# Performance work log

Measured on AMD Instinct MI355X. Metric: run time of the kernel, lower is better.

## Reference

```python
import jax, jax.numpy as jnp
import numpy as np

V = 50000        # fine nodes
E = 400000       # edges
NEXT_DIM = 12500 # coarse nodes (nextDim)
B = 2
FIN, FOUT = 64, 128


def setup_inputs() -> dict:
    key = jax.random.key(0)
    ks = jax.random.split(key, 12)
    x = jax.random.normal(ks[0], (B, V, FIN), dtype=jnp.float32)
    adjValue = jax.random.uniform(ks[1], (E,), dtype=jnp.float32)
    edgeOne = jnp.ones((E,), dtype=jnp.float32)
    E_start = jax.random.randint(ks[2], (E,), 0, V, dtype=jnp.int32)
    E_end = jax.random.randint(ks[3], (E,), 0, V, dtype=jnp.int32)
    # avg-pool assignment: each fine node v -> coarse node v//4, weight 1/4
    fine = jnp.arange(V, dtype=jnp.int32)
    avgPoolAsgnIdx = jnp.stack([fine // 4, fine])  # [2, nnz]
    avgPoolAsgnValue = jnp.full((V,), 0.25, dtype=jnp.float32)
    s = 0.05
    W_res = jax.random.normal(ks[4], (FIN, FOUT), dtype=jnp.float32) * s
    b_res = jnp.zeros((FOUT,), dtype=jnp.float32)
    W0_self = jax.random.normal(ks[5], (FIN, FOUT), dtype=jnp.float32) * s
    W0_nb = jax.random.normal(ks[6], (FIN, FOUT), dtype=jnp.float32) * s
    b0 = jnp.zeros((FOUT,), dtype=jnp.float32)
    W1_self = jax.random.normal(ks[7], (FOUT, FOUT), dtype=jnp.float32) * s
    W1_nb = jax.random.normal(ks[8], (FOUT, FOUT), dtype=jnp.float32) * s
    b1 = jnp.zeros((FOUT,), dtype=jnp.float32)
    return {"x": x, "adjValue": adjValue, "edgeOne": edgeOne,
            "E_start": E_start, "E_end": E_end,
            "avgPoolAsgnIdx": avgPoolAsgnIdx, "avgPoolAsgnValue": avgPoolAsgnValue,
            "W_res": W_res, "b_res": b_res,
            "W0_self": W0_self, "W0_nb": W0_nb, "b0": b0,
            "W1_self": W1_self, "W1_nb": W1_nb, "b1": b1}


def _ecc(x, Ws, Wn, b, adjValue, E_start, E_end, deg_inv):
    # Edge-conditioned conv: out_i = x_i Ws + (1/deg_i) * sum_{e: start=i} adj_e * (x_{end(e)} Wn) + b
    Bn, Vn, _ = x.shape
    h = jnp.einsum('bvf,fo->bvo', x, Wn)            # neighbor transform [B,V,Fo]
    ht = h.transpose(1, 0, 2).reshape(Vn, -1)       # [V, B*Fo]
    msg = ht[E_end] * adjValue[:, None]             # gather + edge weight [E, B*Fo]
    agg = jax.ops.segment_sum(msg, E_start, num_segments=Vn)  # scatter-add [V, B*Fo]
    agg = (agg * deg_inv[:, None]).reshape(Vn, Bn, -1).transpose(1, 0, 2)
    return jnp.einsum('bvf,fo->bvo', x, Ws) + agg + b


def _batch_spmm(idx, value, m, x):
    # sparse (m x n) @ x per batch; x: [B, n, F]
    Bn, n, F = x.shape
    xt = x.transpose(1, 0, 2).reshape(n, -1)        # [n, B*F]
    g = xt[idx[1]] * value[:, None]                 # [nnz, B*F]
    out = jax.ops.segment_sum(g, idx[0], num_segments=m)
    return out.reshape(m, Bn, F).transpose(1, 0, 2)


def reference(x, adjValue, edgeOne, E_start, E_end, avgPoolAsgnIdx, avgPoolAsgnValue,
              W_res, b_res, W0_self, W0_nb, b0, W1_self, W1_nb, b1):
    deg = jax.ops.segment_sum(edgeOne, E_start, num_segments=V)
    deg_inv = 1.0 / jnp.maximum(deg, 1.0)
    # residual path: 1x1 conv == per-node linear, then pool
    residual = jnp.einsum('bvf,fo->bvo', x, W_res) + b_res
    residual = _batch_spmm(avgPoolAsgnIdx, avgPoolAsgnValue, NEXT_DIM, residual)
    # main path: ECC -> leaky_relu(0.2) -> ECC -> pool
    out = _ecc(x, W0_self, W0_nb, b0, adjValue, E_start, E_end, deg_inv)
    out = jnp.where(out >= 0, out, 0.2 * out)
    out = _ecc(out, W1_self, W1_nb, b1, adjValue, E_start, E_end, deg_inv)
    out = _batch_spmm(avgPoolAsgnIdx, avgPoolAsgnValue, NEXT_DIM, out)
    return out + residual
```

## Files before the change

kernel.cpp:

```cpp
#include <hip/hip_runtime.h>

#define V_N    50000
#define E_N    400000
#define NEXT_N 12500
#define B_N    2
#define M_ROWS (V_N * B_N)
#define NSBLK  196

typedef float  f32x2  __attribute__((ext_vector_type(2)));
typedef float  f32x4  __attribute__((ext_vector_type(4)));
typedef __bf16 bf16x8 __attribute__((ext_vector_type(8)));
typedef unsigned int u32x2 __attribute__((ext_vector_type(2)));
typedef unsigned int u32x4 __attribute__((ext_vector_type(4)));

__device__ __forceinline__ float bflo(unsigned int u) {
    return __builtin_bit_cast(float, u << 16);
}
__device__ __forceinline__ float bfhi(unsigned int u) {
    return __builtin_bit_cast(float, u & 0xffff0000u);
}
__device__ __forceinline__ unsigned short bf16bits(float f) {
    return __builtin_bit_cast(unsigned short, (__bf16)f);
}

__device__ __forceinline__ void wcvt_one(int idx, int phase,
                                         const float* Wa, const float* Wb, const float* Wc,
                                         unsigned int* dst) {
    int kc = idx >> 11;
    int jj = idx & 3, lane = (idx >> 2) & 63, nt = (idx >> 8) & 7;
    int kk = kc * 32 + ((lane >> 4) * 8) + jj * 2;
    int n  = nt * 16 + (lane & 15);
    const float* Wsrc; int kbase;
    if (phase == 0) {
        if (kk < 64) { Wsrc = Wa; kbase = 0; } else { Wsrc = Wb; kbase = 64; }
    } else {
        if (kk < 128)      { Wsrc = Wa; kbase = 0; }
        else if (kk < 256) { Wsrc = Wb; kbase = 128; }
        else               { Wsrc = Wc; kbase = 256; }
    }
    float w0 = Wsrc[(kk - kbase) * 128 + n];
    float w1 = Wsrc[(kk + 1 - kbase) * 128 + n];
    dst[idx] = ((unsigned int)bf16bits(w1) << 16) | bf16bits(w0);
}

__global__ void prep_kernel(const float* __restrict__ x, unsigned int* __restrict__ xbf,
                            const int* __restrict__ Es, int* __restrict__ degi,
                            const int* __restrict__ poolIdx, const float* __restrict__ poolVal,
                            int* __restrict__ invRow, float* __restrict__ invVal,
                            const float* __restrict__ W0s, const float* __restrict__ W0n,
                            const float* __restrict__ W1s, const float* __restrict__ W1n,
                            const float* __restrict__ Wres,
                            unsigned int* __restrict__ Wc0, unsigned int* __restrict__ Wc1) {
    int blk = blockIdx.x, t = threadIdx.x;
    if (blk < 12500) {
        int i = blk * 256 + t;
        f32x2 p = *(const f32x2*)(x + (size_t)i * 2);
        xbf[i] = ((unsigned int)bf16bits(p[1]) << 16) | bf16bits(p[0]);
    } else if (blk < 14063) {
        int e = (blk - 12500) * 256 + t;
        if (e < E_N) atomicAdd(&degi[Es[e]], 1);
    } else if (blk < 14259) {
        int j = (blk - 14063) * 256 + t;
        if (j < V_N) {
            int c = poolIdx[V_N + j];
            invRow[c] = poolIdx[j];
            invVal[c] = poolVal[j];
        }
    } else if (blk < 14291) {
        wcvt_one((blk - 14259) * 256 + t, 0, W0s, W0n, nullptr, Wc0);
    } else {
        wcvt_one((blk - 14291) * 256 + t, 1, W1s, W1n, Wres, Wc1);
    }
}

__global__ void partial_kernel(const int* __restrict__ degi, int* __restrict__ part) {
    __shared__ int sh[256];
    int t = threadIdx.x, i = blockIdx.x * 256 + t;
    sh[t] = (i < V_N) ? degi[i] : 0;
    __syncthreads();
    for (int off = 128; off > 0; off >>= 1) {
        if (t < off) sh[t] += sh[t + off];
        __syncthreads();
    }
    if (t == 0) part[blockIdx.x] = sh[0];
}

__global__ void scanpart_kernel(const int* __restrict__ part, int* __restrict__ bofs) {
    __shared__ int sh[256];
    int t = threadIdx.x;
    int p = (t < NSBLK) ? part[t] : 0;
    sh[t] = p;
    __syncthreads();
    for (int off = 1; off < 256; off <<= 1) {
        int v = (t >= off) ? sh[t - off] : 0;
        __syncthreads();
        sh[t] += v;
        __syncthreads();
    }
    if (t < NSBLK) bofs[t] = sh[t] - p;
}

__global__ void emit_kernel(const int* __restrict__ degi, const int* __restrict__ bofs,
                            int* __restrict__ cur, float* __restrict__ dinv) {
    __shared__ int sh[256];
    int t = threadIdx.x, i = blockIdx.x * 256 + t;
    int d = (i < V_N) ? degi[i] : 0;
    sh[t] = d;
    __syncthreads();
    for (int off = 1; off < 256; off <<= 1) {
        int v = (t >= off) ? sh[t - off] : 0;
        __syncthreads();
        sh[t] += v;
        __syncthreads();
    }
    if (i < V_N) {
        cur[i] = bofs[blockIdx.x] + sh[t] - d;
        dinv[i] = 1.0f / (float)(d > 1 ? d : 1);
    }
}

__global__ void csr_kernel(const int* __restrict__ Es, const int* __restrict__ Ee,
                           const float* __restrict__ adj, int* __restrict__ cur,
                           int* __restrict__ cdst, float* __restrict__ cval) {
    int e = blockIdx.x * 256 + threadIdx.x;
    if (e < E_N) {
        int pos = atomicAdd(&cur[Es[e]], 1);
        cdst[pos] = Ee[e];
        cval[pos] = adj[e];
    }
}

__global__ __launch_bounds__(256) void agg0_kernel(
    const unsigned int* __restrict__ xbf, const int* __restrict__ cur,
    const int* __restrict__ cdst, const float* __restrict__ cval,
    const float* __restrict__ dinv, unsigned int* __restrict__ AGG0bf) {
    int w = blockIdx.x * 4 + (threadIdx.x >> 6);
    int lane = threadIdx.x & 63;
    int beg = w ? cur[w - 1] : 0;
    int end = cur[w];
    int b = lane >> 5, u = lane & 31;
    const unsigned int* src = xbf + (size_t)b * V_N * 32 + u;
    float s0 = 0.f, s1 = 0.f;
    for (int base = beg; base < end; base += 8) {
        int li = base + (lane & 7);
        bool lv = li < end;
        int dk = lv ? cdst[li] : 0;
        float ak = lv ? cval[li] : 0.0f;
        unsigned int pv[8]; float av[8];
#pragma unroll
        for (int j = 0; j < 8; ++j) {
            int dj = __shfl(dk, j);
            av[j] = __shfl(ak, j);
            pv[j] = src[(size_t)dj * 32];
        }
#pragma unroll
        for (int j = 0; j < 8; ++j) { s0 += av[j] * bflo(pv[j]); s1 += av[j] * bfhi(pv[j]); }
    }
    float dv = dinv[w];
    AGG0bf[((size_t)b * V_N + w) * 32 + u] =
        ((unsigned int)bf16bits(s1 * dv) << 16) | bf16bits(s0 * dv);
}

__global__ __launch_bounds__(256) void agg1_kernel(
    const unsigned int* __restrict__ obf, const int* __restrict__ cur,
    const int* __restrict__ cdst, const float* __restrict__ cval,
    const float* __restrict__ dinv, unsigned int* __restrict__ AGG1bf) {
    int w = blockIdx.x * 4 + (threadIdx.x >> 6);
    int lane = threadIdx.x & 63;
    int beg = w ? cur[w - 1] : 0;
    int end = cur[w];
    int b = lane >> 5;
    int u = (lane & 31) * 2;
    const unsigned int* src = obf + (size_t)b * V_N * 64 + u;
    float s[4] = {0, 0, 0, 0};
    for (int base = beg; base < end; base += 8) {
        int li = base + (lane & 7);
        bool lv = li < end;
        int dk = lv ? cdst[li] : 0;
        float ak = lv ? cval[li] : 0.0f;
        u32x2 pv[8]; float av[8];
#pragma unroll
        for (int j = 0; j < 8; ++j) {
            int dj = __shfl(dk, j);
            av[j] = __shfl(ak, j);
            pv[j] = *(const u32x2*)(src + (size_t)dj * 64);
        }
#pragma unroll
        for (int j = 0; j < 8; ++j) {
            s[0] += av[j] * bflo(pv[j][0]); s[1] += av[j] * bfhi(pv[j][0]);
            s[2] += av[j] * bflo(pv[j][1]); s[3] += av[j] * bfhi(pv[j][1]);
        }
    }
    float dv = dinv[w];
    u32x2 r;
    r[0] = ((unsigned int)bf16bits(s[1] * dv) << 16) | bf16bits(s[0] * dv);
    r[1] = ((unsigned int)bf16bits(s[3] * dv) << 16) | bf16bits(s[2] * dv);
    *(u32x2*)(AGG1bf + ((size_t)b * V_N + w) * 64 + u) = r;
}

template <int PHASE>
__global__ __launch_bounds__(256) void gemm_kernel(
    const unsigned int* __restrict__ xbf, const unsigned int* __restrict__ INbf,
    const unsigned int* __restrict__ AGGbf, const unsigned int* __restrict__ Wcvt,
    const float* __restrict__ bias0, const float* __restrict__ bias1,
    const int* __restrict__ invRow, const float* __restrict__ invVal,
    unsigned short* __restrict__ OUTbf, float* __restrict__ out) {
    constexpr int K  = (PHASE == 0) ? 128 : 320;
    constexpr int KC = K / 32;

    __shared__ unsigned int ldsW[KC * 2048];

    const int tid  = threadIdx.x;
    const int wave = tid >> 6, lane = tid & 63;
    const int m = lane & 15, quad = lane >> 4;

    {
        const u32x4* src4 = (const u32x4*)Wcvt;
        u32x4* dst4 = (u32x4*)ldsW;
#pragma unroll
        for (int it = 0; it < 2 * KC; ++it) dst4[it * 256 + tid] = src4[it * 256 + tid];
    }
    __syncthreads();

    const int rowA  = blockIdx.x * 64 + wave * 16 + m;
    const int rowAc = rowA < M_ROWS ? rowA : M_ROWS - 1;

    f32x4 acc[8];
#pragma unroll
    for (int i = 0; i < 8; ++i)
#pragma unroll
        for (int r = 0; r < 4; ++r) acc[i][r] = 0.0f;

#pragma unroll
    for (int kc = 0; kc < KC; ++kc) {
        int k0 = kc * 32 + quad * 8;
        const unsigned int* abase;
        if (PHASE == 0) {
            abase = (k0 < 64) ? xbf + (size_t)rowAc * 32 + (k0 >> 1)
                              : AGGbf + (size_t)rowAc * 32 + ((k0 - 64) >> 1);
        } else {
            if (k0 < 128)      abase = INbf + (size_t)rowAc * 64 + (k0 >> 1);
            else if (k0 < 256) abase = AGGbf + (size_t)rowAc * 64 + ((k0 - 128) >> 1);
            else               abase = xbf + (size_t)rowAc * 32 + ((k0 - 256) >> 1);
        }
        bf16x8 av = __builtin_bit_cast(bf16x8, *(const u32x4*)abase);
#pragma unroll
        for (int nt = 0; nt < 8; ++nt) {
            bf16x8 bv = __builtin_bit_cast(
                bf16x8, *(const u32x4*)&ldsW[(kc * 8 + nt) * 256 + lane * 4]);
            acc[nt] = __builtin_amdgcn_mfma_f32_16x16x32_bf16(av, bv, acc[nt], 0, 0, 0);
        }
    }

    const int rowq = blockIdx.x * 64 + wave * 16 + quad * 4;
    if (PHASE == 0) {
#pragma unroll
        for (int nt = 0; nt < 8; ++nt) {
            int o = nt * 16 + m;
            float bias = bias0[o];
#pragma unroll
            for (int r = 0; r < 4; ++r) {
                int orow = rowq + r;
                if (orow < M_ROWS) {
                    float val = acc[nt][r] + bias;
                    val = val >= 0.0f ? val : 0.2f * val;
                    OUTbf[(size_t)orow * 128 + o] = bf16bits(val);
                }
            }
        }
    } else {
        int b = rowq >= V_N;
        int vq = rowq - b * V_N;
        int rr0 = -2, rr1 = -2, rr2 = -2, rr3 = -2;
        float w0 = 0, w1 = 0, w2 = 0, w3 = 0;
        bool inb = (rowq + 3) < M_ROWS;
        if (inb) {
            rr0 = invRow[vq];     w0 = invVal[vq];
            rr1 = invRow[vq + 1]; w1 = invVal[vq + 1];
            rr2 = invRow[vq + 2]; w2 = invVal[vq + 2];
            rr3 = invRow[vq + 3]; w3 = invVal[vq + 3];
        }
        bool uniform = inb && (rr0 >= 0) && (rr0 == rr1) && (rr0 == rr2) && (rr0 == rr3);
#pragma unroll
        for (int nt = 0; nt < 8; ++nt) {
            int o = nt * 16 + m;
            float bias = bias0[o] + bias1[o];
            if (uniform) {
                float pooled = w0 * (acc[nt][0] + bias) + w1 * (acc[nt][1] + bias) +
                               w2 * (acc[nt][2] + bias) + w3 * (acc[nt][3] + bias);
                out[((size_t)b * NEXT_N + rr0) * 128 + o] = pooled;
            } else {
#pragma unroll
                for (int r = 0; r < 4; ++r) {
                    int orow = rowq + r;
                    if (orow < M_ROWS) {
                        int bb = orow >= V_N;
                        int vf = orow - bb * V_N;
                        int rrr = invRow[vf];
                        float www = invVal[vf];
                        if (rrr >= 0)
                            unsafeAtomicAdd(&out[((size_t)bb * NEXT_N + rrr) * 128 + o],
                                            www * (acc[nt][r] + bias));
                    }
                }
            }
        }
    }
}


extern "C" void kernel_launch(void* const* d_in, const int* in_sizes, int n_in,
                              void* d_out, int out_size, void* d_ws, size_t ws_size,
                              hipStream_t stream) {
    const float* x       = (const float*)d_in[0];
    const float* adj     = (const float*)d_in[1];
    const int*   Es      = (const int*)d_in[3];
    const int*   Ee      = (const int*)d_in[4];
    const int*   poolIdx = (const int*)d_in[5];
    const float* poolVal = (const float*)d_in[6];
    const float* W_res   = (const float*)d_in[7];
    const float* b_res   = (const float*)d_in[8];
    const float* W0s     = (const float*)d_in[9];
    const float* W0n     = (const float*)d_in[10];
    const float* b0      = (const float*)d_in[11];
    const float* W1s     = (const float*)d_in[12];
    const float* W1n     = (const float*)d_in[13];
    const float* b1      = (const float*)d_in[14];
    float* out = (float*)d_out;

    char* ws = (char*)d_ws;
    int*   invRow = (int*)  (ws + 0);
    float* invVal = (float*)(ws + 200704);
    int*   degi   = (int*)  (ws + 401408);
    float* dinv   = (float*)(ws + 602112);
    int*   cur    = (int*)  (ws + 802816);
    int*   cdst   = (int*)  (ws + 1003520);
    float* cval   = (float*)(ws + 2604032);
    unsigned int* Wc0 = (unsigned int*)(ws + 4204544);
    unsigned int* Wc1 = (unsigned int*)(ws + 4237312);
    unsigned int* xbf    = (unsigned int*)(ws + 4319232);
    unsigned int* AGG0bf = (unsigned int*)(ws + 17119232);
    unsigned int* OUT0bf = (unsigned int*)(ws + 29919232);
    unsigned int* AGG1bf = (unsigned int*)(ws + 55519232);
    int*   part   = (int*)  (ws + 81119232);
    int*   bofs   = (int*)  (ws + 81120256);

    hipMemsetAsync(degi, 0, (size_t)V_N * 4, stream);
    hipMemsetAsync(invRow, 0xFF, (size_t)V_N * 4, stream);
    hipMemsetAsync(d_out, 0, (size_t)out_size * 4, stream);

    prep_kernel<<<14371, 256, 0, stream>>>(x, xbf, Es, degi, poolIdx, poolVal,
                                           invRow, invVal, W0s, W0n, W1s, W1n, W_res,
                                           Wc0, Wc1);
    partial_kernel<<<NSBLK, 256, 0, stream>>>(degi, part);
    scanpart_kernel<<<1, 256, 0, stream>>>(part, bofs);
    emit_kernel<<<NSBLK, 256, 0, stream>>>(degi, bofs, cur, dinv);
    csr_kernel<<<(E_N + 255) / 256, 256, 0, stream>>>(Es, Ee, adj, cur, cdst, cval);

    agg0_kernel<<<12500, 256, 0, stream>>>(xbf, cur, cdst, cval, dinv, AGG0bf);
    gemm_kernel<0><<<(M_ROWS + 63) / 64, 256, 0, stream>>>(
        xbf, nullptr, AGG0bf, Wc0, b0, nullptr, invRow, invVal,
        (unsigned short*)OUT0bf, nullptr);
    agg1_kernel<<<12500, 256, 0, stream>>>(OUT0bf, cur, cdst, cval, dinv, AGG1bf);
    gemm_kernel<1><<<(M_ROWS + 63) / 64, 256, 0, stream>>>(
        xbf, OUT0bf, AGG1bf, Wc1, b1, b_res, invRow, invVal,
        nullptr, out);
}
```

Before: 252.1 us.

## Fuse degree scan into single-pass decoupled kernel, pack edge data, drop memsets

Replaces the three-kernel prefix scan (partial sums, scan of partials, emit) with one kernel. Each block takes a rank from an atomic counter, publishes its block sum with a release store, and spin-waits on the sums of earlier blocks. Edge destination and weight are packed into one 8-byte struct so the aggregation kernels do one load per edge instead of two. The invRow and output memsets are removed, leaving one memset that also clears the counter and flag array. This cuts launch and memset overhead and some index traffic, but relies on every block being co-resident for the spin-wait, and on invRow and the output being fully written elsewhere.

```diff
diff --git a/kernel.cpp b/kernel.cpp
--- a/kernel.cpp
+++ b/kernel.cpp
@@ -10,6 +10,7 @@
 typedef float  f32x2  __attribute__((ext_vector_type(2)));
 typedef float  f32x4  __attribute__((ext_vector_type(4)));
 typedef __bf16 bf16x8 __attribute__((ext_vector_type(8)));
+typedef int    i32x2  __attribute__((ext_vector_type(2)));
 typedef unsigned int u32x2 __attribute__((ext_vector_type(2)));
 typedef unsigned int u32x4 __attribute__((ext_vector_type(4)));
 
@@ -73,37 +74,19 @@
     }
 }
 
-__global__ void partial_kernel(const int* __restrict__ degi, int* __restrict__ part) {
+__global__ __launch_bounds__(256) void scan_kernel(const int* __restrict__ degi,
+                                                   int* __restrict__ counter,
+                                                   int* __restrict__ aggP,
+                                                   int* __restrict__ cur,
+                                                   float* __restrict__ dinv) {
     __shared__ int sh[256];
-    int t = threadIdx.x, i = blockIdx.x * 256 + t;
-    sh[t] = (i < V_N) ? degi[i] : 0;
+    __shared__ int pref[256];
+    __shared__ int shrank;
+    int t = threadIdx.x;
+    if (t == 0) shrank = atomicAdd(counter, 1);
     __syncthreads();
-    for (int off = 128; off > 0; off >>= 1) {
-        if (t < off) sh[t] += sh[t + off];
-        __syncthreads();
-    }
-    if (t == 0) part[blockIdx.x] = sh[0];
-}
-
-__global__ void scanpart_kernel(const int* __restrict__ part, int* __restrict__ bofs) {
-    __shared__ int sh[256];
-    int t = threadIdx.x;
-    int p = (t < NSBLK) ? part[t] : 0;
-    sh[t] = p;
-    __syncthreads();
-    for (int off = 1; off < 256; off <<= 1) {
-        int v = (t >= off) ? sh[t - off] : 0;
-        __syncthreads();
-        sh[t] += v;
-        __syncthreads();
-    }
-    if (t < NSBLK) bofs[t] = sh[t] - p;
-}
-
-__global__ void emit_kernel(const int* __restrict__ degi, const int* __restrict__ bofs,
-                            int* __restrict__ cur, float* __restrict__ dinv) {
-    __shared__ int sh[256];
-    int t = threadIdx.x, i = blockIdx.x * 256 + t;
+    int rank = shrank;
+    int i = rank * 256 + t;
     int d = (i < V_N) ? degi[i] : 0;
     sh[t] = d;
     __syncthreads();
@@ -113,27 +96,49 @@
         sh[t] += v;
         __syncthreads();
     }
+    int incl = sh[t];
+    int blocksum = sh[255];
+    if (t == 0)
+        __hip_atomic_store(&aggP[rank], blocksum + 1, __ATOMIC_RELEASE,
+                           __HIP_MEMORY_SCOPE_AGENT);
+    int pv = 0;
+    if (t < rank) {
+        int v;
+        do {
+            v = __hip_atomic_load(&aggP[t], __ATOMIC_ACQUIRE, __HIP_MEMORY_SCOPE_AGENT);
+        } while (v == 0);
+        pv = v - 1;
+    }
+    pref[t] = pv;
+    __syncthreads();
+    for (int off = 128; off > 0; off >>= 1) {
+        if (t < off) pref[t] += pref[t + off];
+        __syncthreads();
+    }
+    int prefix = pref[0];
     if (i < V_N) {
-        cur[i] = bofs[blockIdx.x] + sh[t] - d;
+        cur[i] = prefix + incl - d;
         dinv[i] = 1.0f / (float)(d > 1 ? d : 1);
     }
 }
 
 __global__ void csr_kernel(const int* __restrict__ Es, const int* __restrict__ Ee,
                            const float* __restrict__ adj, int* __restrict__ cur,
-                           int* __restrict__ cdst, float* __restrict__ cval) {
+                           i32x2* __restrict__ ecv) {
     int e = blockIdx.x * 256 + threadIdx.x;
     if (e < E_N) {
         int pos = atomicAdd(&cur[Es[e]], 1);
-        cdst[pos] = Ee[e];
-        cval[pos] = adj[e];
+        i32x2 p;
+        p[0] = Ee[e];
+        p[1] = __float_as_int(adj[e]);
+        ecv[pos] = p;
     }
 }
 
 __global__ __launch_bounds__(256) void agg0_kernel(
     const unsigned int* __restrict__ xbf, const int* __restrict__ cur,
-    const int* __restrict__ cdst, const float* __restrict__ cval,
-    const float* __restrict__ dinv, unsigned int* __restrict__ AGG0bf) {
+    const i32x2* __restrict__ ecv, const float* __restrict__ dinv,
+    unsigned int* __restrict__ AGG0bf) {
     int w = blockIdx.x * 4 + (threadIdx.x >> 6);
     int lane = threadIdx.x & 63;
     int beg = w ? cur[w - 1] : 0;
@@ -144,8 +149,10 @@
     for (int base = beg; base < end; base += 8) {
         int li = base + (lane & 7);
         bool lv = li < end;
-        int dk = lv ? cdst[li] : 0;
-        float ak = lv ? cval[li] : 0.0f;
+        i32x2 ev = lv ? ecv[li] : i32x2{0, 0};
+        int dk = ev[0];
+        float ak = __int_as_float(ev[1]);
+        if (!lv) ak = 0.0f;
         unsigned int pv[8]; float av[8];
 #pragma unroll
         for (int j = 0; j < 8; ++j) {
@@ -163,8 +170,8 @@
 
 __global__ __launch_bounds__(256) void agg1_kernel(
     const unsigned int* __restrict__ obf, const int* __restrict__ cur,
-    const int* __restrict__ cdst, const float* __restrict__ cval,
-    const float* __restrict__ dinv, unsigned int* __restrict__ AGG1bf) {
+    const i32x2* __restrict__ ecv, const float* __restrict__ dinv,
+    unsigned int* __restrict__ AGG1bf) {
     int w = blockIdx.x * 4 + (threadIdx.x >> 6);
     int lane = threadIdx.x & 63;
     int beg = w ? cur[w - 1] : 0;
@@ -176,8 +183,10 @@
     for (int base = beg; base < end; base += 8) {
         int li = base + (lane & 7);
         bool lv = li < end;
-        int dk = lv ? cdst[li] : 0;
-        float ak = lv ? cval[li] : 0.0f;
+        i32x2 ev = lv ? ecv[li] : i32x2{0, 0};
+        int dk = ev[0];
+        float ak = __int_as_float(ev[1]);
+        if (!lv) ak = 0.0f;
         u32x2 pv[8]; float av[8];
 #pragma unroll
         for (int j = 0; j < 8; ++j) {
@@ -329,39 +338,34 @@
     float* out = (float*)d_out;
 
     char* ws = (char*)d_ws;
-    int*   invRow = (int*)  (ws + 0);
-    float* invVal = (float*)(ws + 200704);
-    int*   degi   = (int*)  (ws + 401408);
-    float* dinv   = (float*)(ws + 602112);
-    int*   cur    = (int*)  (ws + 802816);
-    int*   cdst   = (int*)  (ws + 1003520);
-    float* cval   = (float*)(ws + 2604032);
-    unsigned int* Wc0 = (unsigned int*)(ws + 4204544);
-    unsigned int* Wc1 = (unsigned int*)(ws + 4237312);
-    unsigned int* xbf    = (unsigned int*)(ws + 4319232);
-    unsigned int* AGG0bf = (unsigned int*)(ws + 17119232);
-    unsigned int* OUT0bf = (unsigned int*)(ws + 29919232);
-    unsigned int* AGG1bf = (unsigned int*)(ws + 55519232);
-    int*   part   = (int*)  (ws + 81119232);
-    int*   bofs   = (int*)  (ws + 81120256);
-
-    hipMemsetAsync(degi, 0, (size_t)V_N * 4, stream);
-    hipMemsetAsync(invRow, 0xFF, (size_t)V_N * 4, stream);
-    hipMemsetAsync(d_out, 0, (size_t)out_size * 4, stream);
+    int*   invRow  = (int*)  (ws + 0);
+    float* invVal  = (float*)(ws + 200704);
+    int*   degi    = (int*)  (ws + 401408);
+    int*   counter = (int*)  (ws + 601408);
+    int*   aggP    = (int*)  (ws + 601412);
+    float* dinv    = (float*)(ws + 602624);
+    int*   cur     = (int*)  (ws + 803328);
+    i32x2* ecv     = (i32x2*)(ws + 1003520);
+    unsigned int* Wc0 = (unsigned int*)(ws + 4203520);
+    unsigned int* Wc1 = (unsigned int*)(ws + 4236288);
+    unsigned int* xbf    = (unsigned int*)(ws + 4318208);
+    unsigned int* AGG0bf = (unsigned int*)(ws + 17118208);
+    unsigned int* OUT0bf = (unsigned int*)(ws + 29918208);
+    unsigned int* AGG1bf = (unsigned int*)(ws + 55518208);
+
+    (void)hipMemsetAsync(degi, 0, 200788, stream);
 
     prep_kernel<<<14371, 256, 0, stream>>>(x, xbf, Es, degi, poolIdx, poolVal,
                                            invRow, invVal, W0s, W0n, W1s, W1n, W_res,
                                            Wc0, Wc1);
-    partial_kernel<<<NSBLK, 256, 0, stream>>>(degi, part);
-    scanpart_kernel<<<1, 256, 0, stream>>>(part, bofs);
-    emit_kernel<<<NSBLK, 256, 0, stream>>>(degi, bofs, cur, dinv);
-    csr_kernel<<<(E_N + 255) / 256, 256, 0, stream>>>(Es, Ee, adj, cur, cdst, cval);
-
-    agg0_kernel<<<12500, 256, 0, stream>>>(xbf, cur, cdst, cval, dinv, AGG0bf);
+    scan_kernel<<<NSBLK, 256, 0, stream>>>(degi, counter, aggP, cur, dinv);
+    csr_kernel<<<(E_N + 255) / 256, 256, 0, stream>>>(Es, Ee, adj, cur, ecv);
+
+    agg0_kernel<<<12500, 256, 0, stream>>>(xbf, cur, ecv, dinv, AGG0bf);
     gemm_kernel<0><<<(M_ROWS + 63) / 64, 256, 0, stream>>>(
         xbf, nullptr, AGG0bf, Wc0, b0, nullptr, invRow, invVal,
         (unsigned short*)OUT0bf, nullptr);
-    agg1_kernel<<<12500, 256, 0, stream>>>(OUT0bf, cur, cdst, cval, dinv, AGG1bf);
+    agg1_kernel<<<12500, 256, 0, stream>>>(OUT0bf, cur, ecv, dinv, AGG1bf);
     gemm_kernel<1><<<(M_ROWS + 63) / 64, 256, 0, stream>>>(
         xbf, OUT0bf, AGG1bf, Wc1, b1, b_res, invRow, invVal,
         nullptr, out);
```

Result: no change. 255.4 us (+1.3%).
